# Kernel tuning notes

Hardware: AMD Instinct MI355X
Metric: run time of the kernel (lower is better)

## Reference

```python
import jax, jax.numpy as jnp
import numpy as np
from functools import partial

EPS = 1e-5
ROPE_THETA = 10000.0
TOP_K = 2


def rmsnorm(x, w):
    # x: [..., d]
    var = jnp.mean(x * x, axis=-1, keepdims=True)
    return x * jax.lax.rsqrt(var + EPS) * w


def apply_rope(x):
    # x: [B, S, H, dh]
    B, S, H, dh = x.shape
    inv_freq = 1.0 / (ROPE_THETA ** (jnp.arange(0, dh, 2, dtype=jnp.float32) / dh))
    ang = jnp.arange(S, dtype=jnp.float32)[:, None] * inv_freq[None, :]  # [S, dh/2]
    cos = jnp.cos(ang)[None, :, None, :]
    sin = jnp.sin(ang)[None, :, None, :]
    x1 = x[..., 0::2]
    x2 = x[..., 1::2]
    r1 = x1 * cos - x2 * sin
    r2 = x1 * sin + x2 * cos
    return jnp.stack([r1, r2], axis=-1).reshape(x.shape)


def setup_inputs() -> dict:
    key = jax.random.key(0)
    B, S, D, H, E = 4, 2048, 512, 8, 8
    Hf = 4 * D  # expert FFN hidden
    ks = jax.random.split(key, 10)
    s = 0.02
    return {
        "x": jax.random.normal(ks[0], (B, S, D), dtype=jnp.float32),
        "attn_norm_w": jnp.ones((D,), dtype=jnp.float32),
        "wq": jax.random.normal(ks[1], (D, D), dtype=jnp.float32) * s,
        "wk": jax.random.normal(ks[2], (D, D), dtype=jnp.float32) * s,
        "wv": jax.random.normal(ks[3], (D, D), dtype=jnp.float32) * s,
        "wo": jax.random.normal(ks[4], (D, D), dtype=jnp.float32) * s,
        "ffn_norm_w": jnp.ones((D,), dtype=jnp.float32),
        "router_w": jax.random.normal(ks[5], (D, E), dtype=jnp.float32) * s,
        "w1": jax.random.normal(ks[6], (E, D, Hf), dtype=jnp.float32) * s,
        "w2": jax.random.normal(ks[7], (E, Hf, D), dtype=jnp.float32) * s,
    }


def mha_rope(xn, wq, wk, wv, wo, num_heads):
    B, S, D = xn.shape
    dh = D // num_heads
    q = (xn @ wq).reshape(B, S, num_heads, dh)
    k = (xn @ wk).reshape(B, S, num_heads, dh)
    v = (xn @ wv).reshape(B, S, num_heads, dh)
    q = apply_rope(q)
    k = apply_rope(k)
    scores = jnp.einsum("bqhd,bkhd->bhqk", q, k) / jnp.sqrt(jnp.float32(dh))
    causal = jnp.tril(jnp.ones((S, S), dtype=bool))
    scores = jnp.where(causal[None, None], scores, jnp.float32(-1e9))
    attn = jax.nn.softmax(scores, axis=-1)
    out = jnp.einsum("bhqk,bkhd->bqhd", attn, v).reshape(B, S, D)
    return out @ wo


def moe_ffn(hn, router_w, w1, w2):
    # hn: [B, S, D] -> tokens [T, D]; top-2 routed expert MLPs (GELU)
    B, S, D = hn.shape
    E = router_w.shape[1]
    t = hn.reshape(B * S, D)
    T = t.shape[0]
    logits = t @ router_w                      # [T, E]
    probs = jax.nn.softmax(logits, axis=-1)
    vals, idx = jax.lax.top_k(probs, TOP_K)    # [T, k]
    gates = vals / jnp.sum(vals, axis=-1, keepdims=True)
    gates_dense = jnp.zeros((T, E), dtype=t.dtype).at[
        jnp.arange(T)[:, None], idx
    ].add(gates)                               # sparse gates, zero for unrouted
    out = jnp.zeros_like(t)
    for e in range(E):  # fixed small expert loop
        ge = gates_dense[:, e:e + 1]           # [T, 1]
        h = jax.nn.gelu(t @ w1[e], approximate=False)
        out = out + ge * (h @ w2[e])
    return out.reshape(B, S, D)


def reference(x, attn_norm_w, wq, wk, wv, wo, ffn_norm_w, router_w, w1, w2):
    num_heads = 8
    h = x + mha_rope(rmsnorm(x, attn_norm_w), wq, wk, wv, wo, num_heads)
    out = h + moe_ffn(rmsnorm(h, ffn_norm_w), router_w, w1, w2)
    return out
```

## Files before the change

kernel.cpp:

```cpp
#include <hip/hip_runtime.h>

#define BATCH 4
#define SEQ 2048
#define DMODEL 512
#define NHEAD 8
#define DHEAD 64
#define NEXP 8
#define DFF 2048
#define TOK (BATCH*SEQ)

typedef __attribute__((ext_vector_type(8))) short short8;
typedef __attribute__((ext_vector_type(8))) _Float16 half8;
typedef __attribute__((ext_vector_type(4))) _Float16 half4;
typedef __attribute__((ext_vector_type(4))) float f32x4;
typedef unsigned short u16;

typedef const __attribute__((address_space(1))) void gvoid;
typedef __attribute__((address_space(3))) void lvoid;
__device__ __forceinline__ void gload16(const void* g, void* l){
  __builtin_amdgcn_global_load_lds((gvoid*)g, (lvoid*)l, 16, 0, 0);
}

__device__ inline f32x4 zero4(){ f32x4 z = {0.f,0.f,0.f,0.f}; return z; }
__device__ inline u16 f2bf(float f){ unsigned u; __builtin_memcpy(&u,&f,4); u = (u + 0x7fffu + ((u>>16)&1u)) >> 16; return (u16)u; }
__device__ inline unsigned pack2(_Float16 a, _Float16 b){
  unsigned short ua, ub; __builtin_memcpy(&ua,&a,2); __builtin_memcpy(&ub,&b,2);
  return (unsigned)ua | ((unsigned)ub<<16);
}

__global__ __launch_bounds__(256) void k_tc_bf(const float* __restrict__ W, u16* __restrict__ Wt, int R, int C){
  __shared__ float tile[32][33];
  long e = blockIdx.z;
  const float* Wp = W + e*(long)R*C;
  u16* Op = Wt + e*(long)R*C;
  int c0 = blockIdx.x*32, r0 = blockIdx.y*32;
  int tx = threadIdx.x & 31, ty = threadIdx.x >> 5;
  #pragma unroll
  for (int i=0;i<4;i++){ int r = ty*4+i; tile[r][tx] = Wp[(long)(r0+r)*C + c0+tx]; }
  __syncthreads();
  #pragma unroll
  for (int i=0;i<4;i++){ int cc = ty*4+i; Op[(long)(c0+cc)*R + r0+tx] = f2bf(tile[tx][cc]); }
}

__global__ __launch_bounds__(256) void k_tc_split(const float* __restrict__ W, _Float16* __restrict__ H, _Float16* __restrict__ L, int R, int C){
  __shared__ float tile[32][33];
  int c0 = blockIdx.x*32, r0 = blockIdx.y*32;
  int tx = threadIdx.x & 31, ty = threadIdx.x >> 5;
  #pragma unroll
  for (int i=0;i<4;i++){ int r = ty*4+i; tile[r][tx] = W[(long)(r0+r)*C + c0+tx]; }
  __syncthreads();
  #pragma unroll
  for (int i=0;i<4;i++){
    int cc = ty*4+i;
    float v = tile[tx][cc];
    _Float16 hi = (_Float16)v;
    long o = (long)(c0+cc)*R + r0+tx;
    H[o] = hi; L[o] = (_Float16)(v - (float)hi);
  }
}

__global__ __launch_bounds__(256) void k_rmsnorm_split(const float* __restrict__ x, const float* __restrict__ w,
                                                       _Float16* __restrict__ oh, _Float16* __restrict__ ol){
  int row = blockIdx.x*4 + (threadIdx.x>>6);
  int lane = threadIdx.x & 63;
  const float4* xr = (const float4*)(x + (long)row*DMODEL);
  float4 a = xr[lane*2], b = xr[lane*2+1];
  float ss = a.x*a.x+a.y*a.y+a.z*a.z+a.w*a.w + b.x*b.x+b.y*b.y+b.z*b.z+b.w*b.w;
  #pragma unroll
  for (int o=32;o;o>>=1) ss += __shfl_xor(ss, o);
  float sc = rsqrtf(ss*(1.0f/DMODEL) + 1e-5f);
  const float4* wr = (const float4*)w;
  float4 wa = wr[lane*2], wb = wr[lane*2+1];
  float v[8] = {a.x*sc*wa.x, a.y*sc*wa.y, a.z*sc*wa.z, a.w*sc*wa.w,
                b.x*sc*wb.x, b.y*sc*wb.y, b.z*sc*wb.z, b.w*sc*wb.w};
  half8 hv, lv;
  #pragma unroll
  for (int j=0;j<8;j++){ _Float16 hi = (_Float16)v[j]; hv[j] = hi; lv[j] = (_Float16)(v[j]-(float)hi); }
  long off = (long)row*DMODEL + lane*8;
  *(half8*)(oh + off) = hv;
  *(half8*)(ol + off) = lv;
}

__global__ __launch_bounds__(256) void k_rope_tab(float2* __restrict__ tab){
  int idx = blockIdx.x*256 + threadIdx.x;
  int s = idx>>5, i = idx&31;
  float invf = powf(10000.0f, -(float)(2*i)*(1.0f/64.0f));
  float ang = (float)s * invf;
  tab[idx] = make_float2(cosf(ang), sinf(ang));
}

template<int EPI>
__global__ __launch_bounds__(256) void k_gemm_split(
    const _Float16* __restrict__ Ah, const _Float16* __restrict__ Al,
    const _Float16* __restrict__ Bh, const _Float16* __restrict__ Bl,
    _Float16* __restrict__ oh, _Float16* __restrict__ ol,
    float* __restrict__ of1, float* __restrict__ of2,
    const float* __restrict__ extra, const float2* __restrict__ tab,
    int M, int N, int K)
{
  __shared__ _Float16 lAb[2*128*64];
  __shared__ _Float16 lBb[2*128*64];
  const int mb = blockIdx.x*128, nb = blockIdx.y*128;
  const int tid = threadIdx.x, lane = tid&63, wv = tid>>6;
  const int wr = wv>>1, wc = wv&1;
  const int fr = lane&15, fq = lane>>4;
  const int cs = (lane&7) ^ (lane>>3);
  const _Float16* pA[4]; const _Float16* pB[4];
  #pragma unroll
  for (int i=0;i<4;i++){
    int rr = i*32 + wv*8 + (lane>>3);
    const _Float16* a = (cs<4)? Ah : Al;
    const _Float16* b = (cs<4)? Bh : Bl;
    pA[i] = a + (long)(mb+rr)*K + (cs&3)*8;
    pB[i] = b + (long)(nb+rr)*K + (cs&3)*8;
  }
  f32x4 acc[4][4];
  #pragma unroll
  for (int mi=0;mi<4;mi++)
    #pragma unroll
    for (int ni=0;ni<4;ni++) acc[mi][ni] = zero4();

  #pragma unroll
  for (int i=0;i<4;i++){
    gload16(pA[i], (char*)lAb + (i*32+wv*8)*128);
    gload16(pB[i], (char*)lBb + (i*32+wv*8)*128);
  }
  __syncthreads();
  const int NT = K>>5;
  int cur = 0;
  for (int t=0; t<NT; ++t){
    if (t+1 < NT){
      int k2 = (t+1)<<5;
      #pragma unroll
      for (int i=0;i<4;i++){
        int db = ((cur^1)<<14) + (i*32+wv*8)*128;
        gload16(pA[i]+k2, (char*)lAb + db);
        gload16(pB[i]+k2, (char*)lBb + db);
      }
    }
    const char* cA = (const char*)lAb + (cur<<14);
    const char* cB = (const char*)lBb + (cur<<14);
    half8 ax[4], ay[4], bx[4], by[4];
    #pragma unroll
    for (int mi=0;mi<4;mi++){
      int row = wr*64 + mi*16 + fr; int m7 = row&7; const char* rb = cA + row*128;
      ax[mi] = *(const half8*)(rb + (((fq  ) ^ m7)<<4));
      ay[mi] = *(const half8*)(rb + (((fq+4) ^ m7)<<4));
    }
    #pragma unroll
    for (int ni=0;ni<4;ni++){
      int row = wc*64 + ni*16 + fr; int m7 = row&7; const char* rb = cB + row*128;
      bx[ni] = *(const half8*)(rb + (((fq  ) ^ m7)<<4));
      by[ni] = *(const half8*)(rb + (((fq+4) ^ m7)<<4));
    }
    __builtin_amdgcn_s_setprio(1);
    #pragma unroll
    for (int mi=0;mi<4;mi++)
      #pragma unroll
      for (int ni=0;ni<4;ni++){
        acc[mi][ni] = __builtin_amdgcn_mfma_f32_16x16x32_f16(ax[mi], bx[ni], acc[mi][ni], 0,0,0);
        acc[mi][ni] = __builtin_amdgcn_mfma_f32_16x16x32_f16(ax[mi], by[ni], acc[mi][ni], 0,0,0);
        acc[mi][ni] = __builtin_amdgcn_mfma_f32_16x16x32_f16(ay[mi], bx[ni], acc[mi][ni], 0,0,0);
      }
    __builtin_amdgcn_s_setprio(0);
    __syncthreads();
    cur ^= 1;
  }
  if (EPI==1){
    #pragma unroll
    for (int mi=0;mi<4;mi++)
      #pragma unroll
      for (int ni=0;ni<4;ni++){
        int row0 = mb + wr*64 + mi*16 + fq*4;
        int col  = nb + wc*64 + ni*16 + fr;
        int d = col & (DHEAD-1), hh = col >> 6;
        int bb = row0 >> 11, s = row0 & (SEQ-1);
        long to = ((long)(bb*NHEAD + hh)*DHEAD + d)*SEQ + s;
        half4 hv, lv;
        #pragma unroll
        for (int r=0;r<4;r++){
          float v = acc[mi][ni][r];
          _Float16 hi = (_Float16)v;
          hv[r] = hi; lv[r] = (_Float16)(v - (float)hi);
        }
        *(half4*)(oh + to) = hv;
        *(half4*)(ol + to) = lv;
      }
  } else {
    #pragma unroll
    for (int mi=0;mi<4;mi++)
      #pragma unroll
      for (int ni=0;ni<4;ni++)
        #pragma unroll
        for (int r=0;r<4;r++){
          int row = mb + wr*64 + mi*16 + fq*4 + r;
          int col = nb + wc*64 + ni*16 + fr;
          long off = (long)row*N + col;
          float v = acc[mi][ni][r];
          if (EPI==0){
            float v2 = __shfl_xor(v, 1);
            float2 csn = tab[(row & (SEQ-1))*32 + ((col&63)>>1)];
            float o = (col&1) ? (v2*csn.y + v*csn.x) : (v*csn.x - v2*csn.y);
            _Float16 hi = (_Float16)o;
            oh[off] = hi; ol[off] = (_Float16)(o - (float)hi);
          } else {
            float hv = extra[off] + v;
            of1[off] = hv; of2[off] = hv;
          }
        }
  }
}

__global__ __launch_bounds__(256) void k_flash(
    const _Float16* __restrict__ Qh, const _Float16* __restrict__ Ql,
    const _Float16* __restrict__ Kh, const _Float16* __restrict__ Kl,
    const _Float16* __restrict__ Vth, const _Float16* __restrict__ Vtl,
    _Float16* __restrict__ Oh, _Float16* __restrict__ Ol)
{
  __shared__ _Float16 lK[64*128];
  __shared__ _Float16 lV[64*128];
  __shared__ _Float16 lP[4*2304];
  const int pidx = blockIdx.x, bh = blockIdx.y;
  const int b = bh>>3, hh = bh&7;
  const int tid = threadIdx.x, lane = tid&63, wid = tid>>6;
  const int fr = lane&15, fq = lane>>4;
  const long base = ((long)b*SEQ)*DMODEL + hh*DHEAD;
  const long vtb  = (long)bh*DHEAD*SEQ;
  const int srow = tid>>4, sch = tid&15;
  const unsigned pw = wid*2304;
  const float SCL = 0.18033688011112042f;

  half8 kreg[4], vreg[4];
  const _Float16* ks = (sch<8) ? Kh : Kl;
  const _Float16* vs = (sch<8) ? Vth : Vtl;
  #pragma unroll
  for (int i=0;i<4;i++){
    int row = i*16 + srow;
    kreg[i] = *(const half8*)(ks + base + (long)row*DMODEL + (sch&7)*8);
    vreg[i] = *(const half8*)(vs + vtb + (long)row*SEQ + (sch&7)*8);
  }

  for (int pass=0; pass<2; pass++){
    const int qt = pass ? (SEQ/64-1-pidx) : pidx;
    const int q0 = qt*64, qw = q0 + wid*16;
    half8 qfh[2], qfl[2];
    #pragma unroll
    for (int kk=0;kk<2;kk++){
      long o = base + (long)(qw+fr)*DMODEL + kk*32 + fq*8;
      qfh[kk] = *(const half8*)(Qh + o);
      qfl[kk] = *(const half8*)(Ql + o);
    }
    f32x4 oacc[4];
    #pragma unroll
    for (int i=0;i<4;i++) oacc[i] = zero4();
    float mrow[4], lrow[4];
    #pragma unroll
    for (int r=0;r<4;r++){ mrow[r] = -__builtin_inff(); lrow[r] = 0.f; }

    for (int kvt=0; kvt<=qt; kvt++){
      int k0 = kvt*64;
      __syncthreads();
      #pragma unroll
      for (int i=0;i<4;i++){
        int row = i*16 + srow;
        int slot = ((sch ^ (row&15))<<4);
        *(half8*)((char*)lK + row*256 + slot) = kreg[i];
        *(half8*)((char*)lV + row*256 + slot) = vreg[i];
      }
      __syncthreads();
      {
        int nk0 = -1;
        if (kvt < qt) nk0 = k0 + 64;
        else if (pass == 0) nk0 = 0;
        if (nk0 >= 0){
          #pragma unroll
          for (int i=0;i<4;i++){
            int row = i*16 + srow;
            kreg[i] = *(const half8*)(ks + base + (long)(nk0+row)*DMODEL + (sch&7)*8);
            vreg[i] = *(const half8*)(vs + vtb + (long)row*SEQ + nk0 + (sch&7)*8);
          }
        }
      }
      f32x4 sc[4];
      __builtin_amdgcn_s_setprio(1);
      #pragma unroll
      for (int ns=0;ns<4;ns++){
        f32x4 a = zero4();
        #pragma unroll
        for (int kk=0;kk<2;kk++){
          int row = ns*16 + fr; int m15 = row&15; const char* rb = (const char*)lK + row*256;
          half8 kfh = *(const half8*)(rb + (((kk*4+fq)   ^ m15)<<4));
          half8 kfl = *(const half8*)(rb + (((kk*4+fq+8) ^ m15)<<4));
          a = __builtin_amdgcn_mfma_f32_16x16x32_f16(qfh[kk], kfh, a, 0,0,0);
          a = __builtin_amdgcn_mfma_f32_16x16x32_f16(qfh[kk], kfl, a, 0,0,0);
          a = __builtin_amdgcn_mfma_f32_16x16x32_f16(qfl[kk], kfh, a, 0,0,0);
        }
        sc[ns] = a;
      }
      __builtin_amdgcn_s_setprio(0);
      float pmax[4];
      #pragma unroll
      for (int r=0;r<4;r++) pmax[r] = -__builtin_inff();
      if (kvt == qt){
        #pragma unroll
        for (int ns=0;ns<4;ns++)
          #pragma unroll
          for (int r=0;r<4;r++){
            int kvp = k0 + ns*16 + fr;
            int qp  = qw + fq*4 + r;
            float s = sc[ns][r]*SCL;
            if (kvp > qp) s = -1e30f;
            sc[ns][r] = s;
            pmax[r] = fmaxf(pmax[r], s);
          }
      } else {
        #pragma unroll
        for (int ns=0;ns<4;ns++)
          #pragma unroll
          for (int r=0;r<4;r++){
            float s = sc[ns][r]*SCL;
            sc[ns][r] = s;
            pmax[r] = fmaxf(pmax[r], s);
          }
      }
      #pragma unroll
      for (int o=1;o<16;o<<=1)
        #pragma unroll
        for (int r=0;r<4;r++) pmax[r] = fmaxf(pmax[r], __shfl_xor(pmax[r], o));
      bool need = false;
      #pragma unroll
      for (int r=0;r<4;r++) need = need || (pmax[r] > mrow[r] + 10.f);
      if (__any(need)){
        float sf[4];
        #pragma unroll
        for (int r=0;r<4;r++){
          float mn = fmaxf(mrow[r], pmax[r]);
          sf[r] = exp2f(mrow[r]-mn);
          mrow[r] = mn;
          lrow[r] *= sf[r];
        }
        #pragma unroll
        for (int dt=0;dt<4;dt++)
          #pragma unroll
          for (int r=0;r<4;r++) oacc[dt][r] *= sf[r];
      }
      float rsum[4] = {0,0,0,0};
      #pragma unroll
      for (int ns=0;ns<4;ns++)
        #pragma unroll
        for (int r=0;r<4;r++){
          float pv = exp2f(sc[ns][r]-mrow[r]);
          rsum[r] += pv;
          float pv2 = __shfl_xor(pv, 1);
          float e0 = (fr&1)? pv2 : pv;
          float e1 = (fr&1)? pv : pv2;
          _Float16 f0 = (_Float16)e0, f1 = (_Float16)e1;
          unsigned word;
          if (fr&1) word = pack2((_Float16)(e0-(float)f0), (_Float16)(e1-(float)f1));
          else      word = pack2(f0, f1);
          unsigned eo = pw + ((fr&1)? 1152u:0u) + (unsigned)((fq*4+r)*72 + ns*16 + (fr&~1));
          *(unsigned*)((char*)lP + eo*2) = word;
        }
      #pragma unroll
      for (int o=1;o<16;o<<=1)
        #pragma unroll
        for (int r=0;r<4;r++) rsum[r] += __shfl_xor(rsum[r], o);
      #pragma unroll
      for (int r=0;r<4;r++) lrow[r] += rsum[r];
      __builtin_amdgcn_s_setprio(1);
      #pragma unroll
      for (int kk=0;kk<2;kk++){
        const char* pb = (const char*)lP + (pw + (unsigned)(fr*72 + kk*32))*2;
        half8 pfh = *(const half8*)(pb + fq*16);
        half8 pfl = *(const half8*)(pb + 2304 + fq*16);
        #pragma unroll
        for (int dt=0;dt<4;dt++){
          int row = dt*16 + fr; int m15 = row&15; const char* vb = (const char*)lV + row*256;
          half8 vfh = *(const half8*)(vb + (((kk*4+fq)   ^ m15)<<4));
          half8 vfl = *(const half8*)(vb + (((kk*4+fq+8) ^ m15)<<4));
          oacc[dt] = __builtin_amdgcn_mfma_f32_16x16x32_f16(pfh, vfh, oacc[dt], 0,0,0);
          oacc[dt] = __builtin_amdgcn_mfma_f32_16x16x32_f16(pfh, vfl, oacc[dt], 0,0,0);
          oacc[dt] = __builtin_amdgcn_mfma_f32_16x16x32_f16(pfl, vfh, oacc[dt], 0,0,0);
        }
      }
      __builtin_amdgcn_s_setprio(0);
    }
    #pragma unroll
    for (int dt=0;dt<4;dt++)
      #pragma unroll
      for (int r=0;r<4;r++){
        int qp = qw + fq*4 + r;
        float ov = oacc[dt][r] / lrow[r];
        long o = base + (long)qp*DMODEL + dt*16 + fr;
        _Float16 hi = (_Float16)ov;
        Oh[o] = hi; Ol[o] = (_Float16)(ov - (float)hi);
      }
  }
}

__global__ __launch_bounds__(256) void k_router(const float* __restrict__ h, const float* __restrict__ w,
                                                const float* __restrict__ rw, float* __restrict__ gates,
                                                unsigned* __restrict__ choice, u16* __restrict__ hnb){
  int tok = blockIdx.x*4 + (threadIdx.x>>6);
  int lane = threadIdx.x & 63;
  const float4* xr = (const float4*)(h + (long)tok*DMODEL);
  float4 a = xr[lane*2], b = xr[lane*2+1];
  float ss = a.x*a.x+a.y*a.y+a.z*a.z+a.w*a.w + b.x*b.x+b.y*b.y+b.z*b.z+b.w*b.w;
  #pragma unroll
  for (int o=32;o;o>>=1) ss += __shfl_xor(ss, o);
  float sc = rsqrtf(ss*(1.0f/DMODEL) + 1e-5f);
  const float4* wr = (const float4*)w;
  float4 wa = wr[lane*2], wb = wr[lane*2+1];
  float xv[8] = {a.x*sc*wa.x, a.y*sc*wa.y, a.z*sc*wa.z, a.w*sc*wa.w,
                 b.x*sc*wb.x, b.y*sc*wb.y, b.z*sc*wb.z, b.w*sc*wb.w};
  short8 ov;
  #pragma unroll
  for (int j=0;j<8;j++) ov[j] = (short)f2bf(xv[j]);
  *(short8*)(hnb + (long)tok*DMODEL + lane*8) = ov;
  float lg[8] = {0,0,0,0,0,0,0,0};
  #pragma unroll
  for (int j=0;j<8;j++){
    const float* rp = rw + (long)(lane*8+j)*NEXP;
    #pragma unroll
    for (int e=0;e<8;e++) lg[e] += xv[j]*rp[e];
  }
  #pragma unroll
  for (int o=1;o<64;o<<=1)
    #pragma unroll
    for (int e=0;e<8;e++) lg[e] += __shfl_xor(lg[e], o);
  float mx = lg[0];
  #pragma unroll
  for (int e=1;e<8;e++) mx = fmaxf(mx, lg[e]);
  float pe[8], sm = 0.f;
  #pragma unroll
  for (int e=0;e<8;e++){ pe[e] = expf(lg[e]-mx); sm += pe[e]; }
  #pragma unroll
  for (int e=0;e<8;e++) pe[e] /= sm;
  int e1 = 0; float p1 = pe[0];
  #pragma unroll
  for (int e=1;e<8;e++) if (pe[e] > p1){ p1 = pe[e]; e1 = e; }
  int e2 = -1; float p2 = -1.f;
  #pragma unroll
  for (int e=0;e<8;e++) if (e != e1 && pe[e] > p2){ p2 = pe[e]; e2 = e; }
  float gs = p1 + p2;
  if (lane == 0){
    #pragma unroll
    for (int e=0;e<8;e++)
      gates[(long)tok*NEXP + e] = (e==e1) ? (p1/gs) : ((e==e2) ? (p2/gs) : 0.f);
    choice[tok] = (unsigned)e1 | ((unsigned)e2<<8);
  }
}

__global__ __launch_bounds__(256) void k_build(const unsigned* __restrict__ choice,
                                               int* __restrict__ cnt, int* __restrict__ perm){
  __shared__ int lcnt[NEXP];
  __shared__ int lbase[NEXP];
  const int tid = threadIdx.x;
  const int tok = blockIdx.x*256 + tid;
  if (tid < NEXP) lcnt[tid] = 0;
  __syncthreads();
  unsigned ch = choice[tok];
  int e1 = ch & 0xff, e2 = (ch>>8) & 0xff;
  int p1 = atomicAdd(&lcnt[e1], 1);
  int p2 = atomicAdd(&lcnt[e2], 1);
  __syncthreads();
  if (tid < NEXP) lbase[tid] = atomicAdd(&cnt[tid], lcnt[tid]);
  __syncthreads();
  perm[e1*TOK + lbase[e1] + p1] = tok;
  perm[e2*TOK + lbase[e2] + p2] = tok;
}

__global__ void k_prefix(const int* __restrict__ cnt, int* __restrict__ baseP){
  if (threadIdx.x==0 && blockIdx.x==0){
    int run = 0;
    for (int e=0;e<NEXP;e++){ baseP[e] = run; run += (cnt[e]+127) & ~127; }
  }
}

__global__ __launch_bounds__(256) void k_moe1(
    const u16* __restrict__ A, const u16* __restrict__ W1, u16* __restrict__ mid,
    const int* __restrict__ perm, const int* __restrict__ cnt, const int* __restrict__ baseP)
{
  const int e = blockIdx.z;
  const int ce = cnt[e];
  const int mb = blockIdx.x*128;
  if (mb >= ce) return;
  const int bp = baseP[e];
  const u16* Bt = W1 + (size_t)e*DFF*DMODEL;
  const int nb = blockIdx.y*128;
  __shared__ u16 lA[128*64];
  __shared__ u16 lB[128*64];
  const int tid = threadIdx.x, lane = tid&63, wv = tid>>6;
  const int wr = wv>>1, wc = wv&1;
  const int fr = lane&15, fq = lane>>4;
  const int cs = (lane&7) ^ (lane>>3);
  const u16* pA[4]; const u16* pB[4];
  #pragma unroll
  for (int i=0;i<4;i++){
    int rr = mb + i*32 + wv*8 + (lane>>3);
    int tok = perm[e*TOK + (rr < ce ? rr : ce-1)];
    pA[i] = A  + (long)tok*DMODEL + cs*8;
    pB[i] = Bt + (long)(nb + i*32 + wv*8 + (lane>>3))*DMODEL + cs*8;
  }
  f32x4 acc[4][4];
  #pragma unroll
  for (int mi=0;mi<4;mi++)
    #pragma unroll
    for (int ni=0;ni<4;ni++) acc[mi][ni] = zero4();

  for (int kt=0; kt<DMODEL; kt+=64){
    #pragma unroll
    for (int i=0;i<4;i++){
      gload16(pA[i]+kt, (char*)lA + (i*32+wv*8)*128);
      gload16(pB[i]+kt, (char*)lB + (i*32+wv*8)*128);
    }
    __syncthreads();
    __builtin_amdgcn_s_setprio(1);
    #pragma unroll
    for (int kk=0;kk<2;kk++){
      short8 af[4], bff[4];
      #pragma unroll
      for (int mi=0;mi<4;mi++){
        int row = wr*64 + mi*16 + fr;
        af[mi] = *(const short8*)((char*)lA + row*128 + (((kk*4+fq) ^ (row&7))<<4));
      }
      #pragma unroll
      for (int ni=0;ni<4;ni++){
        int row = wc*64 + ni*16 + fr;
        bff[ni] = *(const short8*)((char*)lB + row*128 + (((kk*4+fq) ^ (row&7))<<4));
      }
      #pragma unroll
      for (int mi=0;mi<4;mi++)
        #pragma unroll
        for (int ni=0;ni<4;ni++)
          acc[mi][ni] = __builtin_amdgcn_mfma_f32_16x16x32_bf16(af[mi], bff[ni], acc[mi][ni], 0,0,0);
    }
    __builtin_amdgcn_s_setprio(0);
    __syncthreads();
  }
  #pragma unroll
  for (int mi=0;mi<4;mi++)
    #pragma unroll
    for (int ni=0;ni<4;ni++)
      #pragma unroll
      for (int r=0;r<4;r++){
        int row_loc = mb + wr*64 + mi*16 + fq*4 + r;
        int col = nb + wc*64 + ni*16 + fr;
        float v = acc[mi][ni][r];
        mid[(size_t)(bp + row_loc)*DFF + col] = f2bf(0.5f*v*(1.f + erff(v*0.7071067811865475f)));
      }
}

__global__ __launch_bounds__(256) void k_moe2(
    const u16* __restrict__ mid, const u16* __restrict__ W2, float* __restrict__ out,
    const int* __restrict__ perm, const int* __restrict__ cnt, const int* __restrict__ baseP,
    const float* __restrict__ gates)
{
  const int ez = blockIdx.z;
  const int e = ez>>1, kh = ez&1;
  const int ce = cnt[e];
  const int mb = blockIdx.x*128;
  if (mb >= ce) return;
  const int bp = baseP[e];
  const u16* Bt = W2 + (size_t)e*DMODEL*DFF;
  const int nb = blockIdx.y*128;
  __shared__ u16 lA[128*64];
  __shared__ u16 lB[128*64];
  const int tid = threadIdx.x, lane = tid&63, wv = tid>>6;
  const int wr = wv>>1, wc = wv&1;
  const int fr = lane&15, fq = lane>>4;
  const int cs = (lane&7) ^ (lane>>3);
  const u16* pA[4]; const u16* pB[4];
  #pragma unroll
  for (int i=0;i<4;i++){
    int rr = i*32 + wv*8 + (lane>>3);
    pA[i] = mid + (size_t)(bp + mb + rr)*DFF + cs*8;
    pB[i] = Bt  + (long)(nb + rr)*DFF + cs*8;
  }
  f32x4 acc[4][4];
  #pragma unroll
  for (int mi=0;mi<4;mi++)
    #pragma unroll
    for (int ni=0;ni<4;ni++) acc[mi][ni] = zero4();

  const int kbeg = kh*(DFF/2), kend = kbeg + DFF/2;
  for (int kt=kbeg; kt<kend; kt+=64){
    #pragma unroll
    for (int i=0;i<4;i++){
      gload16(pA[i]+kt, (char*)lA + (i*32+wv*8)*128);
      gload16(pB[i]+kt, (char*)lB + (i*32+wv*8)*128);
    }
    __syncthreads();
    __builtin_amdgcn_s_setprio(1);
    #pragma unroll
    for (int kk=0;kk<2;kk++){
      short8 af[4], bff[4];
      #pragma unroll
      for (int mi=0;mi<4;mi++){
        int row = wr*64 + mi*16 + fr;
        af[mi] = *(const short8*)((char*)lA + row*128 + (((kk*4+fq) ^ (row&7))<<4));
      }
      #pragma unroll
      for (int ni=0;ni<4;ni++){
        int row = wc*64 + ni*16 + fr;
        bff[ni] = *(const short8*)((char*)lB + row*128 + (((kk*4+fq) ^ (row&7))<<4));
      }
      #pragma unroll
      for (int mi=0;mi<4;mi++)
        #pragma unroll
        for (int ni=0;ni<4;ni++)
          acc[mi][ni] = __builtin_amdgcn_mfma_f32_16x16x32_bf16(af[mi], bff[ni], acc[mi][ni], 0,0,0);
    }
    __builtin_amdgcn_s_setprio(0);
    __syncthreads();
  }
  #pragma unroll
  for (int mi=0;mi<4;mi++)
    #pragma unroll
    for (int ni=0;ni<4;ni++)
      #pragma unroll
      for (int r=0;r<4;r++){
        int row_loc = mb + wr*64 + mi*16 + fq*4 + r;
        if (row_loc < ce){
          int tok = perm[e*TOK + row_loc];
          int col = nb + wc*64 + ni*16 + fr;
          float g = gates[(long)tok*NEXP + e];
          atomicAdd(out + (long)tok*DMODEL + col, g*acc[mi][ni][r]);
        }
      }
}

extern "C" void kernel_launch(void* const* d_in, const int* in_sizes, int n_in,
                              void* d_out, int out_size, void* d_ws, size_t ws_size,
                              hipStream_t stream)
{
  const float* x   = (const float*)d_in[0];
  const float* anw = (const float*)d_in[1];
  const float* wq  = (const float*)d_in[2];
  const float* wk  = (const float*)d_in[3];
  const float* wv  = (const float*)d_in[4];
  const float* wo  = (const float*)d_in[5];
  const float* fnw = (const float*)d_in[6];
  const float* rw  = (const float*)d_in[7];
  const float* w1  = (const float*)d_in[8];
  const float* w2  = (const float*)d_in[9];
  float* out = (float*)d_out;

  char* p = (char*)d_ws;
  auto alloc = [&](size_t n){ char* r = p; p += (n + 255) & ~(size_t)255; return r; };
  _Float16* xnh = (_Float16*)alloc((size_t)TOK*DMODEL*2);
  _Float16* xnl = (_Float16*)alloc((size_t)TOK*DMODEL*2);
  _Float16* qh  = (_Float16*)alloc((size_t)TOK*DMODEL*2);
  _Float16* ql  = (_Float16*)alloc((size_t)TOK*DMODEL*2);
  _Float16* kh  = (_Float16*)alloc((size_t)TOK*DMODEL*2);
  _Float16* kl  = (_Float16*)alloc((size_t)TOK*DMODEL*2);
  _Float16* vth = (_Float16*)alloc((size_t)TOK*DMODEL*2);
  _Float16* vtl = (_Float16*)alloc((size_t)TOK*DMODEL*2);
  _Float16* pad1 = (_Float16*)alloc((size_t)TOK*DMODEL*2);
  _Float16* pad2 = (_Float16*)alloc((size_t)TOK*DMODEL*2);
  (void)pad1; (void)pad2;
  u16* hmid = (u16*)xnh;
  _Float16* wqTh = (_Float16*)alloc((size_t)DMODEL*DMODEL*2);
  _Float16* wqTl = (_Float16*)alloc((size_t)DMODEL*DMODEL*2);
  _Float16* wkTh = (_Float16*)alloc((size_t)DMODEL*DMODEL*2);
  _Float16* wkTl = (_Float16*)alloc((size_t)DMODEL*DMODEL*2);
  _Float16* wvTh = (_Float16*)alloc((size_t)DMODEL*DMODEL*2);
  _Float16* wvTl = (_Float16*)alloc((size_t)DMODEL*DMODEL*2);
  _Float16* woTh = (_Float16*)alloc((size_t)DMODEL*DMODEL*2);
  _Float16* woTl = (_Float16*)alloc((size_t)DMODEL*DMODEL*2);
  u16* w1T = (u16*)alloc((size_t)NEXP*DFF*DMODEL*2);
  u16* w2T = (u16*)alloc((size_t)NEXP*DMODEL*DFF*2);
  _Float16* aoh = (_Float16*)alloc((size_t)TOK*DMODEL*2);
  _Float16* aol = (_Float16*)alloc((size_t)TOK*DMODEL*2);
  float* hb  = (float*)alloc((size_t)TOK*DMODEL*4);
  u16* hnb   = (u16*)alloc((size_t)TOK*DMODEL*2);
  float2* tab = (float2*)alloc((size_t)SEQ*32*sizeof(float2));
  float* gates = (float*)alloc((size_t)TOK*NEXP*4);
  int* perm  = (int*)alloc((size_t)NEXP*TOK*4);
  unsigned* choice = (unsigned*)alloc((size_t)TOK*4);
  int* cnt   = (int*)alloc(64*4);
  int* baseP = (int*)alloc(64*4);

  dim3 blk(256);
  hipMemsetAsync(cnt, 0, NEXP*sizeof(int), stream);
  k_tc_split<<<dim3(16,16,1), blk, 0, stream>>>(wq, wqTh, wqTl, DMODEL, DMODEL);
  k_tc_split<<<dim3(16,16,1), blk, 0, stream>>>(wk, wkTh, wkTl, DMODEL, DMODEL);
  k_tc_split<<<dim3(16,16,1), blk, 0, stream>>>(wv, wvTh, wvTl, DMODEL, DMODEL);
  k_tc_split<<<dim3(16,16,1), blk, 0, stream>>>(wo, woTh, woTl, DMODEL, DMODEL);
  k_tc_bf<<<dim3(DFF/32, DMODEL/32, NEXP), blk, 0, stream>>>(w1, w1T, DMODEL, DFF);
  k_tc_bf<<<dim3(DMODEL/32, DFF/32, NEXP), blk, 0, stream>>>(w2, w2T, DFF, DMODEL);
  k_rope_tab<<<dim3(SEQ*32/256), blk, 0, stream>>>(tab);
  k_rmsnorm_split<<<dim3(TOK/4), blk, 0, stream>>>(x, anw, xnh, xnl);
  k_gemm_split<0><<<dim3(TOK/128, DMODEL/128), blk, 0, stream>>>(xnh, xnl, wqTh, wqTl, qh, ql, nullptr, nullptr, nullptr, tab, TOK, DMODEL, DMODEL);
  k_gemm_split<0><<<dim3(TOK/128, DMODEL/128), blk, 0, stream>>>(xnh, xnl, wkTh, wkTl, kh, kl, nullptr, nullptr, nullptr, tab, TOK, DMODEL, DMODEL);
  k_gemm_split<1><<<dim3(TOK/128, DMODEL/128), blk, 0, stream>>>(xnh, xnl, wvTh, wvTl, vth, vtl, nullptr, nullptr, nullptr, nullptr, TOK, DMODEL, DMODEL);
  k_flash<<<dim3(SEQ/128, BATCH*NHEAD), blk, 0, stream>>>(qh, ql, kh, kl, vth, vtl, aoh, aol);
  k_gemm_split<2><<<dim3(TOK/128, DMODEL/128), blk, 0, stream>>>(aoh, aol, woTh, woTl, nullptr, nullptr, hb, out, x, nullptr, TOK, DMODEL, DMODEL);
  k_router<<<dim3(TOK/4), blk, 0, stream>>>(hb, fnw, rw, gates, choice, hnb);
  k_build<<<dim3(TOK/256), blk, 0, stream>>>(choice, cnt, perm);
  k_prefix<<<dim3(1), dim3(64), 0, stream>>>(cnt, baseP);
  k_moe1<<<dim3(TOK/128, DFF/128, NEXP), blk, 0, stream>>>(hnb, w1T, hmid, perm, cnt, baseP);
  k_moe2<<<dim3(TOK/128, DMODEL/128, NEXP*2), blk, 0, stream>>>(hmid, w2T, out, perm, cnt, baseP, gates);
}
```

Baseline: 752.9 us.

## Replace MoE down-proj atomics with per-slot bf16 outputs and combine kernel

```diff
diff --git a/kernel.cpp b/kernel.cpp
--- a/kernel.cpp
+++ b/kernel.cpp
@@ -23,6 +23,7 @@
 
 __device__ inline f32x4 zero4(){ f32x4 z = {0.f,0.f,0.f,0.f}; return z; }
 __device__ inline u16 f2bf(float f){ unsigned u; __builtin_memcpy(&u,&f,4); u = (u + 0x7fffu + ((u>>16)&1u)) >> 16; return (u16)u; }
+__device__ inline float bf2f(u16 s){ unsigned u = ((unsigned)s)<<16; float f; __builtin_memcpy(&f,&u,4); return f; }
 __device__ inline unsigned pack2(_Float16 a, _Float16 b){
   unsigned short ua, ub; __builtin_memcpy(&ua,&a,2); __builtin_memcpy(&ub,&b,2);
   return (unsigned)ua | ((unsigned)ub<<16);
@@ -94,7 +95,7 @@
     const _Float16* __restrict__ Ah, const _Float16* __restrict__ Al,
     const _Float16* __restrict__ Bh, const _Float16* __restrict__ Bl,
     _Float16* __restrict__ oh, _Float16* __restrict__ ol,
-    float* __restrict__ of1, float* __restrict__ of2,
+    float* __restrict__ of1,
     const float* __restrict__ extra, const float2* __restrict__ tab,
     int M, int N, int K)
 {
@@ -204,8 +205,7 @@
             _Float16 hi = (_Float16)o;
             oh[off] = hi; ol[off] = (_Float16)(o - (float)hi);
           } else {
-            float hv = extra[off] + v;
-            of1[off] = hv; of2[off] = hv;
+            of1[off] = extra[off] + v;
           }
         }
   }
@@ -552,20 +552,19 @@
 }
 
 __global__ __launch_bounds__(256) void k_moe2(
-    const u16* __restrict__ mid, const u16* __restrict__ W2, float* __restrict__ out,
+    const u16* __restrict__ mid, const u16* __restrict__ W2, u16* __restrict__ y,
     const int* __restrict__ perm, const int* __restrict__ cnt, const int* __restrict__ baseP,
-    const float* __restrict__ gates)
+    const unsigned* __restrict__ choice)
 {
-  const int ez = blockIdx.z;
-  const int e = ez>>1, kh = ez&1;
+  const int e = blockIdx.z;
   const int ce = cnt[e];
   const int mb = blockIdx.x*128;
   if (mb >= ce) return;
   const int bp = baseP[e];
   const u16* Bt = W2 + (size_t)e*DMODEL*DFF;
   const int nb = blockIdx.y*128;
-  __shared__ u16 lA[128*64];
-  __shared__ u16 lB[128*64];
+  __shared__ u16 lA[2*128*64];
+  __shared__ u16 lB[2*128*64];
   const int tid = threadIdx.x, lane = tid&63, wv = tid>>6;
   const int wr = wv>>1, wc = wv&1;
   const int fr = lane&15, fq = lane>>4;
@@ -583,14 +582,26 @@
     #pragma unroll
     for (int ni=0;ni<4;ni++) acc[mi][ni] = zero4();
 
-  const int kbeg = kh*(DFF/2), kend = kbeg + DFF/2;
-  for (int kt=kbeg; kt<kend; kt+=64){
-    #pragma unroll
-    for (int i=0;i<4;i++){
-      gload16(pA[i]+kt, (char*)lA + (i*32+wv*8)*128);
-      gload16(pB[i]+kt, (char*)lB + (i*32+wv*8)*128);
-    }
-    __syncthreads();
+  #pragma unroll
+  for (int i=0;i<4;i++){
+    gload16(pA[i], (char*)lA + (i*32+wv*8)*128);
+    gload16(pB[i], (char*)lB + (i*32+wv*8)*128);
+  }
+  __syncthreads();
+  const int NT = DFF/64;
+  int cur = 0;
+  for (int t=0; t<NT; ++t){
+    if (t+1 < NT){
+      int k2 = (t+1)*64;
+      #pragma unroll
+      for (int i=0;i<4;i++){
+        int db = ((cur^1)<<14) + (i*32+wv*8)*128;
+        gload16(pA[i]+k2, (char*)lA + db);
+        gload16(pB[i]+k2, (char*)lB + db);
+      }
+    }
+    const char* cA = (const char*)lA + (cur<<14);
+    const char* cB = (const char*)lB + (cur<<14);
     __builtin_amdgcn_s_setprio(1);
     #pragma unroll
     for (int kk=0;kk<2;kk++){
@@ -598,12 +609,12 @@
       #pragma unroll
       for (int mi=0;mi<4;mi++){
         int row = wr*64 + mi*16 + fr;
-        af[mi] = *(const short8*)((char*)lA + row*128 + (((kk*4+fq) ^ (row&7))<<4));
+        af[mi] = *(const short8*)(cA + row*128 + (((kk*4+fq) ^ (row&7))<<4));
       }
       #pragma unroll
       for (int ni=0;ni<4;ni++){
         int row = wc*64 + ni*16 + fr;
-        bff[ni] = *(const short8*)((char*)lB + row*128 + (((kk*4+fq) ^ (row&7))<<4));
+        bff[ni] = *(const short8*)(cB + row*128 + (((kk*4+fq) ^ (row&7))<<4));
       }
       #pragma unroll
       for (int mi=0;mi<4;mi++)
@@ -613,6 +624,7 @@
     }
     __builtin_amdgcn_s_setprio(0);
     __syncthreads();
+    cur ^= 1;
   }
   #pragma unroll
   for (int mi=0;mi<4;mi++)
@@ -623,11 +635,35 @@
         int row_loc = mb + wr*64 + mi*16 + fq*4 + r;
         if (row_loc < ce){
           int tok = perm[e*TOK + row_loc];
+          int k = (e == (int)(choice[tok] & 0xffu)) ? 0 : 1;
           int col = nb + wc*64 + ni*16 + fr;
-          float g = gates[(long)tok*NEXP + e];
-          atomicAdd(out + (long)tok*DMODEL + col, g*acc[mi][ni][r]);
+          y[((long)tok*2 + k)*DMODEL + col] = f2bf(acc[mi][ni][r]);
         }
       }
+}
+
+__global__ __launch_bounds__(256) void k_combine(const float* __restrict__ hb, const u16* __restrict__ y,
+                                                 const float* __restrict__ gates, const unsigned* __restrict__ choice,
+                                                 float* __restrict__ out){
+  int tok = blockIdx.x*4 + (threadIdx.x>>6);
+  int lane = threadIdx.x & 63;
+  unsigned ch = choice[tok];
+  int e1 = ch & 0xff, e2 = (ch>>8) & 0xff;
+  float g1 = gates[(long)tok*NEXP + e1];
+  float g2 = gates[(long)tok*NEXP + e2];
+  const float4* h4 = (const float4*)(hb + (long)tok*DMODEL);
+  short8 u = *(const short8*)(y + ((long)tok*2    )*DMODEL + lane*8);
+  short8 v = *(const short8*)(y + ((long)tok*2 + 1)*DMODEL + lane*8);
+  float4* o4 = (float4*)(out + (long)tok*DMODEL);
+  #pragma unroll
+  for (int j=0;j<2;j++){
+    float4 a = h4[lane*2+j];
+    a.x += g1*bf2f((u16)u[j*4+0]) + g2*bf2f((u16)v[j*4+0]);
+    a.y += g1*bf2f((u16)u[j*4+1]) + g2*bf2f((u16)v[j*4+1]);
+    a.z += g1*bf2f((u16)u[j*4+2]) + g2*bf2f((u16)v[j*4+2]);
+    a.w += g1*bf2f((u16)u[j*4+3]) + g2*bf2f((u16)v[j*4+3]);
+    o4[lane*2+j] = a;
+  }
 }
 
 extern "C" void kernel_launch(void* const* d_in, const int* in_sizes, int n_in,
@@ -672,6 +708,7 @@
   u16* w2T = (u16*)alloc((size_t)NEXP*DMODEL*DFF*2);
   _Float16* aoh = (_Float16*)alloc((size_t)TOK*DMODEL*2);
   _Float16* aol = (_Float16*)alloc((size_t)TOK*DMODEL*2);
+  u16* yexp = (u16*)aoh;
   float* hb  = (float*)alloc((size_t)TOK*DMODEL*4);
   u16* hnb   = (u16*)alloc((size_t)TOK*DMODEL*2);
   float2* tab = (float2*)alloc((size_t)SEQ*32*sizeof(float2));
@@ -691,14 +728,15 @@
   k_tc_bf<<<dim3(DMODEL/32, DFF/32, NEXP), blk, 0, stream>>>(w2, w2T, DFF, DMODEL);
   k_rope_tab<<<dim3(SEQ*32/256), blk, 0, stream>>>(tab);
   k_rmsnorm_split<<<dim3(TOK/4), blk, 0, stream>>>(x, anw, xnh, xnl);
-  k_gemm_split<0><<<dim3(TOK/128, DMODEL/128), blk, 0, stream>>>(xnh, xnl, wqTh, wqTl, qh, ql, nullptr, nullptr, nullptr, tab, TOK, DMODEL, DMODEL);
-  k_gemm_split<0><<<dim3(TOK/128, DMODEL/128), blk, 0, stream>>>(xnh, xnl, wkTh, wkTl, kh, kl, nullptr, nullptr, nullptr, tab, TOK, DMODEL, DMODEL);
-  k_gemm_split<1><<<dim3(TOK/128, DMODEL/128), blk, 0, stream>>>(xnh, xnl, wvTh, wvTl, vth, vtl, nullptr, nullptr, nullptr, nullptr, TOK, DMODEL, DMODEL);
+  k_gemm_split<0><<<dim3(TOK/128, DMODEL/128), blk, 0, stream>>>(xnh, xnl, wqTh, wqTl, qh, ql, nullptr, nullptr, tab, TOK, DMODEL, DMODEL);
+  k_gemm_split<0><<<dim3(TOK/128, DMODEL/128), blk, 0, stream>>>(xnh, xnl, wkTh, wkTl, kh, kl, nullptr, nullptr, tab, TOK, DMODEL, DMODEL);
+  k_gemm_split<1><<<dim3(TOK/128, DMODEL/128), blk, 0, stream>>>(xnh, xnl, wvTh, wvTl, vth, vtl, nullptr, nullptr, nullptr, TOK, DMODEL, DMODEL);
   k_flash<<<dim3(SEQ/128, BATCH*NHEAD), blk, 0, stream>>>(qh, ql, kh, kl, vth, vtl, aoh, aol);
-  k_gemm_split<2><<<dim3(TOK/128, DMODEL/128), blk, 0, stream>>>(aoh, aol, woTh, woTl, nullptr, nullptr, hb, out, x, nullptr, TOK, DMODEL, DMODEL);
+  k_gemm_split<2><<<dim3(TOK/128, DMODEL/128), blk, 0, stream>>>(aoh, aol, woTh, woTl, nullptr, nullptr, hb, x, nullptr, TOK, DMODEL, DMODEL);
   k_router<<<dim3(TOK/4), blk, 0, stream>>>(hb, fnw, rw, gates, choice, hnb);
   k_build<<<dim3(TOK/256), blk, 0, stream>>>(choice, cnt, perm);
   k_prefix<<<dim3(1), dim3(64), 0, stream>>>(cnt, baseP);
   k_moe1<<<dim3(TOK/128, DFF/128, NEXP), blk, 0, stream>>>(hnb, w1T, hmid, perm, cnt, baseP);
-  k_moe2<<<dim3(TOK/128, DMODEL/128, NEXP*2), blk, 0, stream>>>(hmid, w2T, out, perm, cnt, baseP, gates);
-}
+  k_moe2<<<dim3(TOK/128, DMODEL/128, NEXP), blk, 0, stream>>>(hmid, w2T, yexp, perm, cnt, baseP, choice);
+  k_combine<<<dim3(TOK/4), blk, 0, stream>>>(hb, yexp, gates, choice, out);
+}
```

Result: faster. 694.8 us (-7.7%).
